# Performance work log

Measured on AMD Instinct MI355X. Metric: run time of the kernel, lower is better.

Reference implementation:

```python
import jax, jax.numpy as jnp
import numpy as np

NUM_HEAD = 8
D_K = 64


def setup_inputs() -> dict:
    key = jax.random.key(0)
    k1, k2, k3 = jax.random.split(key, 3)
    B, S, D = 8, 1024, 512
    input_x = jax.random.normal(k1, (B, S, D), dtype=jnp.float32)
    W_qkv = jax.random.normal(k2, (D, 3 * D), dtype=jnp.float32) * 0.02
    W_out = jax.random.normal(k3, (D, D), dtype=jnp.float32) * 0.02
    return {"input_x": input_x, "W_qkv": W_qkv, "W_out": W_out}


def reference(input_x, W_qkv, W_out):
    B, S, D = input_x.shape
    H, dk = NUM_HEAD, D_K
    qkv = input_x @ W_qkv  # (B, S, 3*D)
    # Faithful to the source: per-head slices OVERLAP.
    # head h: Q=qkv[h*dk:(h+1)*dk], K=qkv[(h+1)*dk:(h+2)*dk], V=qkv[(h+2)*dk:(h+3)*dk]
    Q = qkv[:, :, 0:H * dk].reshape(B, S, H, dk)
    K = qkv[:, :, dk:dk + H * dk].reshape(B, S, H, dk)
    V = qkv[:, :, 2 * dk:2 * dk + H * dk].reshape(B, S, H, dk)
    scale = jnp.asarray(1.0 / np.sqrt(dk), dtype=qkv.dtype)
    scores = jnp.einsum('bqhd,bkhd->bhqk', Q, K) * scale  # (B, H, S, S)
    # nn.Softmax() with dim=None on a 3D (B,S,S) tensor -> legacy dim=0 (batch axis)
    attn = jax.nn.softmax(scores, axis=0)
    out = jnp.einsum('bhqk,bkhd->bqhd', attn, V).reshape(B, S, H * dk)
    return out @ W_out
```

## Files before the change

### kernel.cpp

```cpp
#include <hip/hip_runtime.h>

typedef __bf16 bf16x8 __attribute__((ext_vector_type(8)));
typedef float  f32x4  __attribute__((ext_vector_type(4)));
typedef unsigned short u16x8 __attribute__((ext_vector_type(8)));
typedef unsigned short USHORT;

__device__ __forceinline__ USHORT f2bf(float f) {
    unsigned u = __float_as_uint(f);
    u += 0x7fffu + ((u >> 16) & 1u);
    return (USHORT)(u >> 16);
}

__device__ __forceinline__ float bf2f(USHORT v) {
    return __uint_as_float((unsigned)v << 16);
}

__device__ __forceinline__ f32x4 fz4() { f32x4 z = {0.f, 0.f, 0.f, 0.f}; return z; }

__device__ __forceinline__ bf16x8 ldbf8(const USHORT* p) { return *(const bf16x8*)p; }

__device__ __forceinline__ f32x4 mfma16(bf16x8 a, bf16x8 b, f32x4 c) {
    return __builtin_amdgcn_mfma_f32_16x16x32_bf16(a, b, c, 0, 0, 0);
}

__device__ __forceinline__ void gload_lds16(const void* g, void* s) {
    __builtin_amdgcn_global_load_lds(
        (const __attribute__((address_space(1))) unsigned int*)g,
        (__attribute__((address_space(3))) unsigned int*)s, 16, 0, 0);
}

__device__ __forceinline__ void lds_fence() {
    asm volatile("s_waitcnt lgkmcnt(0)" ::: "memory");
    __builtin_amdgcn_sched_barrier(0);
}

__global__ __launch_bounds__(256) void prep_kernel(const float* __restrict__ X,
                                                   const float* __restrict__ Wqkv,
                                                   const float* __restrict__ Wout,
                                                   USHORT* __restrict__ Xb,
                                                   USHORT* __restrict__ Wt1,
                                                   USHORT* __restrict__ Wt3) {
    int bid = blockIdx.x;
    if (bid < 2048) {
        int base = (bid * 256 + threadIdx.x) * 8;
        float4 a = *(const float4*)(X + base);
        float4 b = *(const float4*)(X + base + 4);
        u16x8 o;
        o[0] = f2bf(a.x); o[1] = f2bf(a.y); o[2] = f2bf(a.z); o[3] = f2bf(a.w);
        o[4] = f2bf(b.x); o[5] = f2bf(b.y); o[6] = f2bf(b.z); o[7] = f2bf(b.w);
        *(u16x8*)(Xb + base) = o;
    } else if (bid < 3328) {
        int t = (bid - 2048) * 256 + threadIdx.x;
        int k = t & 511, n = t >> 9;
        Wt1[t] = f2bf(Wqkv[(size_t)k * 1536 + n]);
    } else {
        int t = (bid - 3328) * 256 + threadIdx.x;
        int k = t & 511, n = t >> 9;
        Wt3[t] = f2bf(Wout[(size_t)k * 512 + n]);
    }
}

__global__ __launch_bounds__(256) void reduce2(const USHORT* __restrict__ a,
                                               const USHORT* __restrict__ b,
                                               USHORT* __restrict__ o) {
    int base = (blockIdx.x * 256 + threadIdx.x) * 8;
    u16x8 va = *(const u16x8*)(a + base);
    u16x8 vb = *(const u16x8*)(b + base);
    u16x8 out;
#pragma unroll
    for (int j = 0; j < 8; ++j)
        out[j] = f2bf(bf2f(va[j]) + bf2f(vb[j]));
    *(u16x8*)(o + base) = out;
}

template <bool BF16OUT>
__global__ __launch_bounds__(256) void gemm_bt(const USHORT* __restrict__ A,
                                               const USHORT* __restrict__ Bt,
                                               void* __restrict__ Cv,
                                               int M, int N, int K) {
    __shared__ __align__(16) USHORT Asm[128 * 32];
    __shared__ __align__(16) USHORT Bsm[128 * 32];
    const int tid = threadIdx.x;
    const int wv = tid >> 6, ln = tid & 63;
    const int l16 = ln & 15, quad = ln >> 4;
    const int m0 = blockIdx.x * 128, n0 = blockIdx.y * 128;
    const int wm = (wv >> 1) * 64, wn = (wv & 1) * 64;

    f32x4 acc[4][4];
#pragma unroll
    for (int i = 0; i < 4; ++i)
#pragma unroll
        for (int j = 0; j < 4; ++j) acc[i][j] = fz4();

    const int kTiles = K >> 5;
    for (int kt = 0; kt < kTiles; ++kt) {
        __syncthreads();
#pragma unroll
        for (int i = 0; i < 2; ++i) {
            int cb = wv * 128 + i * 64;
            int c = cb + ln;
            gload_lds16(A + (size_t)(m0 + (c >> 2)) * K + kt * 32 + (c & 3) * 8,
                        &Asm[cb * 8]);
            gload_lds16(Bt + (size_t)(n0 + (c >> 2)) * K + kt * 32 + (c & 3) * 8,
                        &Bsm[cb * 8]);
        }
        __syncthreads();

        bf16x8 af[4], bfr[4];
#pragma unroll
        for (int i = 0; i < 4; ++i)
            af[i] = ldbf8(&Asm[(wm + i * 16 + l16) * 32 + quad * 8]);
#pragma unroll
        for (int j = 0; j < 4; ++j)
            bfr[j] = ldbf8(&Bsm[(wn + j * 16 + l16) * 32 + quad * 8]);
#pragma unroll
        for (int i = 0; i < 4; ++i)
#pragma unroll
            for (int j = 0; j < 4; ++j)
                acc[i][j] = mfma16(af[i], bfr[j], acc[i][j]);
    }

#pragma unroll
    for (int i = 0; i < 4; ++i)
#pragma unroll
        for (int j = 0; j < 4; ++j)
#pragma unroll
            for (int r = 0; r < 4; ++r) {
                size_t row = m0 + wm + i * 16 + quad * 4 + r;
                size_t col = n0 + wn + j * 16 + l16;
                if (BF16OUT)
                    ((USHORT*)Cv)[row * N + col] = f2bf(acc[i][j][r]);
                else
                    ((float*)Cv)[row * N + col] = acc[i][j][r];
            }
}

__global__ __launch_bounds__(256) void transpose_v(const USHORT* __restrict__ P,
                                                   USHORT* __restrict__ Vt) {
    __shared__ __align__(16) USHORT T[64][72];
    const int t = threadIdx.x;
    const int k0 = blockIdx.x * 64;
    const int hh = blockIdx.y;
    const int b = blockIdx.z;
#pragma unroll
    for (int i = 0; i < 2; ++i) {
        int c = i * 256 + t;
        int kk = c >> 3, d8 = (c & 7) * 8;
        u16x8 v = *(const u16x8*)(P + (size_t)((b << 10) + k0 + kk) * 640 +
                                  (hh + 2) * 64 + d8);
        *(u16x8*)&T[kk][d8] = v;
    }
    __syncthreads();
#pragma unroll
    for (int i = 0; i < 2; ++i) {
        int d = (t >> 3) + i * 32;
        int kk0 = (t & 7) * 8;
        u16x8 v;
#pragma unroll
        for (int j = 0; j < 8; ++j) v[j] = T[kk0 + j][d];
        *(u16x8*)(Vt + (size_t)(((b << 3) + hh) * 64 + d) * 1024 + k0 + kk0) = v;
    }
}

__global__ __launch_bounds__(256, 1) void attn_kernel(const USHORT* __restrict__ P,
                                                      const USHORT* __restrict__ Vt,
                                                      USHORT* __restrict__ pt0,
                                                      USHORT* __restrict__ pt1) {
    const int bid = blockIdx.x;
    const int g = bid & 15;
    const int h = g >> 1;
    const int kc = g & 1;
    const int qb = bid >> 4;
    const int tid = threadIdx.x;
    const int wv = tid >> 6;
    const int lane = tid & 63;
    const int l16 = lane & 15, quad = lane >> 4;
    const int q0 = qb * 64 + wv * 16;

    __shared__ __align__(16) USHORT Kl[2][16384];
    __shared__ __align__(16) USHORT Vl[2][16384];
    __shared__ __align__(16) USHORT alds[2048];
    USHORT* mytile = &alds[wv * 512];

    const int hi = l16 >> 3;
    const int cq = quad * 4 + (hi << 4);
    const int xq = (quad >> 1) | (hi << 1);
    const int boff = (l16 & 7) * 2;
    const int rdoff = (lane ^ ((lane >> 3) & 7)) << 4;

    bf16x8 qf[8][2];
#pragma unroll
    for (int b = 0; b < 8; ++b)
#pragma unroll
        for (int ks = 0; ks < 2; ++ks)
            qf[b][ks] = ldbf8(P + (size_t)((b << 10) + q0 + l16) * 640 + h * 64 +
                              ks * 32 + quad * 8);

    f32x4 oacc[8][4];
#pragma unroll
    for (int b = 0; b < 8; ++b)
#pragma unroll
        for (int nt = 0; nt < 4; ++nt) oacc[b][nt] = fz4();

    auto stage = [&](int k0s, int buf) {
        if (wv < 2) {
#pragma unroll
            for (int i = 0; i < 16; ++i) {
                int gg = wv * 16 + i;
                int b = gg >> 2, ks = (gg >> 1) & 1, half = gg & 1;
                gload_lds16(P + (size_t)((b << 10) + k0s + half * 16 + (lane & 15)) * 640 +
                                (h + 1) * 64 + ks * 32 + (lane >> 4) * 8,
                            &Kl[buf][(b * 2 + ks) * 1024 + half * 512]);
            }
        } else {
#pragma unroll
            for (int i = 0; i < 16; ++i) {
                int gg = (wv - 2) * 16 + i;
                int b = gg >> 2, dq = gg & 3;
                gload_lds16(Vt + (size_t)(((b << 3) + h) * 64 + dq * 16 + (lane & 15)) * 1024 +
                                k0s + (lane >> 4) * 8,
                            &Vl[buf][b * 2048 + dq * 512]);
            }
        }
    };

    const int kbase = kc * 512;
    stage(kbase, 0);
    __syncthreads();

    int buf = 0;
    for (int it = 0; it < 16; ++it) {
        if (it < 15) stage(kbase + (it + 1) * 32, buf ^ 1);

        const USHORT* Kb = Kl[buf];
        const USHORT* Vb = Vl[buf];

        f32x4 sacc[8][2];
#pragma unroll
        for (int b = 0; b < 8; ++b) { sacc[b][0] = fz4(); sacc[b][1] = fz4(); }
#pragma unroll
        for (int ks = 0; ks < 2; ++ks)
#pragma unroll
            for (int nt = 0; nt < 2; ++nt) {
                bf16x8 kf[8];
#pragma unroll
                for (int b = 0; b < 8; ++b)
                    kf[b] = ldbf8(&Kb[(b * 2 + ks) * 1024 + nt * 512 + lane * 8]);
#pragma unroll
                for (int b = 0; b < 8; ++b)
                    sacc[b][nt] = mfma16(qf[b][ks], kf[b], sacc[b][nt]);
            }

#pragma unroll
        for (int nt = 0; nt < 2; ++nt)
#pragma unroll
            for (int r = 0; r < 4; ++r) {
                float e[8];
                float Z = 0.f;
#pragma unroll
                for (int b = 0; b < 8; ++b) {
                    e[b] = __builtin_amdgcn_exp2f(sacc[b][nt][r] * 0.1803368801f);
                    Z += e[b];
                }
                float inv = __builtin_amdgcn_rcpf(Z);
#pragma unroll
                for (int b = 0; b < 8; ++b)
                    sacc[b][nt][r] = e[b] * inv;
            }

#pragma unroll
        for (int b = 0; b < 8; ++b) {
#pragma unroll
            for (int nt = 0; nt < 2; ++nt)
#pragma unroll
                for (int r = 0; r < 4; ++r) {
                    int c = cq | r | (nt << 5);
                    int x = xq | (nt << 2);
                    int off = (((c ^ x) << 4) | boff);
                    *(USHORT*)((char*)mytile + off) = f2bf(sacc[b][nt][r]);
                }
            lds_fence();

            bf16x8 af = *(const bf16x8*)((const char*)mytile + rdoff);
            bf16x8 vf[4];
#pragma unroll
            for (int nt = 0; nt < 4; ++nt)
                vf[nt] = ldbf8(&Vb[b * 2048 + nt * 512 + lane * 8]);
#pragma unroll
            for (int nt = 0; nt < 4; ++nt)
                oacc[b][nt] = mfma16(af, vf[nt], oacc[b][nt]);
            lds_fence();
        }

        __syncthreads();
        buf ^= 1;
    }

    USHORT* part = kc ? pt1 : pt0;
    USHORT* ep = ((USHORT*)Kl) + wv * (16 * 72);
#pragma unroll
    for (int b = 0; b < 8; ++b) {
#pragma unroll
        for (int nt = 0; nt < 4; ++nt)
#pragma unroll
            for (int r = 0; r < 4; ++r)
                ep[(quad * 4 + r) * 72 + nt * 16 + l16] = f2bf(oacc[b][nt][r]);
        lds_fence();
#pragma unroll
        for (int half = 0; half < 2; ++half) {
            int row = half * 8 + (lane >> 3);
            int seg = lane & 7;
            u16x8 v = *(const u16x8*)&ep[row * 72 + seg * 8];
            *(u16x8*)(part + (size_t)((b << 10) + q0 + row) * 512 + h * 64 + seg * 8) = v;
        }
        lds_fence();
    }
}

extern "C" void kernel_launch(void* const* d_in, const int* in_sizes, int n_in,
                              void* d_out, int out_size, void* d_ws, size_t ws_size,
                              hipStream_t stream) {
    const float* X = (const float*)d_in[0];
    const float* Wqkv = (const float*)d_in[1];
    const float* Wout = (const float*)d_in[2];
    float* out = (float*)d_out;

    char* w = (char*)d_ws;
    USHORT* Xb  = (USHORT*)(w);
    USHORT* Wt1 = (USHORT*)(w + 8388608);
    USHORT* Wt3 = (USHORT*)(w + 9043968);
    USHORT* P   = (USHORT*)(w + 9568256);
    USHORT* Vt  = (USHORT*)(w + 20054016);
    USHORT* pt1 = (USHORT*)(w + 28442624);
    USHORT* pt0 = Xb;
    USHORT* CtxB = Xb;

    prep_kernel<<<4352, 256, 0, stream>>>(X, Wqkv, Wout, Xb, Wt1, Wt3);
    gemm_bt<true><<<dim3(64, 5), 256, 0, stream>>>(Xb, Wt1, (void*)P, 8192, 640, 512);
    transpose_v<<<dim3(16, 8, 8), 256, 0, stream>>>(P, Vt);
    attn_kernel<<<256, 256, 0, stream>>>(P, Vt, pt0, pt1);
    reduce2<<<2048, 256, 0, stream>>>(pt0, pt1, CtxB);
    gemm_bt<false><<<dim3(64, 4), 256, 0, stream>>>(CtxB, Wt3, (void*)out, 8192, 512, 512);
}
```

Baseline: 188.4 us.

## Transpose score MFMAs and redistribute P via ds_permute instead of LDS round-trip

Swaps the MFMA operand order so the score and output accumulators come out transposed. Softmax probabilities are packed into bf16 pairs and redistributed across lanes with ds_permute and selects, replacing the per-batch LDS scatter/gather and its two lgkm fences. The epilogue store indexing is adjusted for the transposed output layout. This removes shared-memory traffic and serialising waits from the inner loop, at the cost of extra permute and select instructions.

```diff
diff --git a/kernel.cpp b/kernel.cpp
--- a/kernel.cpp
+++ b/kernel.cpp
@@ -4,6 +4,7 @@
 typedef float  f32x4  __attribute__((ext_vector_type(4)));
 typedef unsigned short u16x8 __attribute__((ext_vector_type(8)));
 typedef unsigned short USHORT;
+typedef unsigned int   u32;
 
 __device__ __forceinline__ USHORT f2bf(float f) {
     unsigned u = __float_as_uint(f);
@@ -13,6 +14,10 @@
 
 __device__ __forceinline__ float bf2f(USHORT v) {
     return __uint_as_float((unsigned)v << 16);
+}
+
+__device__ __forceinline__ u32 packbf(float lo, float hi) {
+    return (u32)f2bf(lo) | ((u32)f2bf(hi) << 16);
 }
 
 __device__ __forceinline__ f32x4 fz4() { f32x4 z = {0.f, 0.f, 0.f, 0.f}; return z; }
@@ -179,14 +184,12 @@
 
     __shared__ __align__(16) USHORT Kl[2][16384];
     __shared__ __align__(16) USHORT Vl[2][16384];
-    __shared__ __align__(16) USHORT alds[2048];
-    USHORT* mytile = &alds[wv * 512];
-
-    const int hi = l16 >> 3;
-    const int cq = quad * 4 + (hi << 4);
-    const int xq = (quad >> 1) | (hi << 1);
-    const int boff = (l16 & 7) * 2;
-    const int rdoff = (lane ^ ((lane >> 3) & 7)) << 4;
+
+    const int qhalf = quad >> 1;
+    const bool qodd = (quad & 1) != 0;
+    const bool qhi  = quad >= 2;
+    const int idx01 = ((qodd ? (2 + qhalf) : qhalf) * 16 + l16) * 4;
+    const int idx23 = ((qodd ? qhalf : (2 + qhalf)) * 16 + l16) * 4;
 
     bf16x8 qf[8][2];
 #pragma unroll
@@ -248,7 +251,7 @@
                     kf[b] = ldbf8(&Kb[(b * 2 + ks) * 1024 + nt * 512 + lane * 8]);
 #pragma unroll
                 for (int b = 0; b < 8; ++b)
-                    sacc[b][nt] = mfma16(qf[b][ks], kf[b], sacc[b][nt]);
+                    sacc[b][nt] = mfma16(kf[b], qf[b][ks], sacc[b][nt]);
             }
 
 #pragma unroll
@@ -270,26 +273,30 @@
 
 #pragma unroll
         for (int b = 0; b < 8; ++b) {
-#pragma unroll
-            for (int nt = 0; nt < 2; ++nt)
-#pragma unroll
-                for (int r = 0; r < 4; ++r) {
-                    int c = cq | r | (nt << 5);
-                    int x = xq | (nt << 2);
-                    int off = (((c ^ x) << 4) | boff);
-                    *(USHORT*)((char*)mytile + off) = f2bf(sacc[b][nt][r]);
-                }
-            lds_fence();
-
-            bf16x8 af = *(const bf16x8*)((const char*)mytile + rdoff);
+            u32 w00 = packbf(sacc[b][0][0], sacc[b][0][1]);
+            u32 w01 = packbf(sacc[b][0][2], sacc[b][0][3]);
+            u32 w10 = packbf(sacc[b][1][0], sacc[b][1][1]);
+            u32 w11 = packbf(sacc[b][1][2], sacc[b][1][3]);
+            u32 s0 = qodd ? w10 : w00, s1 = qodd ? w11 : w01;
+            u32 s2 = qodd ? w00 : w10, s3 = qodd ? w01 : w11;
+            u32 r0 = (u32)__builtin_amdgcn_ds_permute(idx01, (int)s0);
+            u32 r1 = (u32)__builtin_amdgcn_ds_permute(idx01, (int)s1);
+            u32 r2 = (u32)__builtin_amdgcn_ds_permute(idx23, (int)s2);
+            u32 r3 = (u32)__builtin_amdgcn_ds_permute(idx23, (int)s3);
+            union { u32 u[4]; bf16x8 v; } pu;
+            pu.u[0] = qhi ? r2 : r0;
+            pu.u[1] = qhi ? r3 : r1;
+            pu.u[2] = qhi ? r0 : r2;
+            pu.u[3] = qhi ? r1 : r3;
+            bf16x8 pb = pu.v;
+
             bf16x8 vf[4];
 #pragma unroll
             for (int nt = 0; nt < 4; ++nt)
                 vf[nt] = ldbf8(&Vb[b * 2048 + nt * 512 + lane * 8]);
 #pragma unroll
             for (int nt = 0; nt < 4; ++nt)
-                oacc[b][nt] = mfma16(af, vf[nt], oacc[b][nt]);
-            lds_fence();
+                oacc[b][nt] = mfma16(vf[nt], pb, oacc[b][nt]);
         }
 
         __syncthreads();
@@ -304,7 +311,7 @@
         for (int nt = 0; nt < 4; ++nt)
 #pragma unroll
             for (int r = 0; r < 4; ++r)
-                ep[(quad * 4 + r) * 72 + nt * 16 + l16] = f2bf(oacc[b][nt][r]);
+                ep[l16 * 72 + nt * 16 + quad * 4 + r] = f2bf(oacc[b][nt][r]);
         lds_fence();
 #pragma unroll
         for (int half = 0; half < 2; ++half) {
```

Result: faster. 175.7 us (-6.7%).
